# Kernel optimization log

Hardware: AMD Instinct MI355X
Metric: run time of the kernel (lower is better)

The kernel has to match this reference:

```python
import jax, jax.numpy as jnp
import numpy as np

N, H_IN, W_IN, D_OUT = 4, 512, 360, 512


def _ramp_filter(H):
    # fourier_fbp_filter(..., 'ramp') -> time domain, fftshifted, then reversed
    f = np.fft.fftfreq(H).reshape(-1, 1)
    fourier_filter = 2.0 * np.abs(f)
    time_filter = np.fft.fftshift(np.fft.ifft(fourier_filter, axis=0).real)
    time_filter = time_filter[::-1].copy()  # list-reverse in the original
    return time_filter.reshape(1, 1, H, 1).astype(np.float32)  # OIHW


def _backproj_ty(H, W, D):
    # y-coordinate of the grid_sample grid; x-coordinate exactly selects column i
    th = np.pi / 180.0 * np.linspace(0.0, 180.0, W, endpoint=False)  # [W]
    X, Y = np.mgrid[0:D, 0:D]
    xpr = (X - D // 2).astype(np.float64)
    ypr = (Y - D // 2).astype(np.float64)
    t = ypr[None] * np.cos(th)[:, None, None] - xpr[None] * np.sin(th)[:, None, None]
    return (t / (H // 2)).astype(np.float32)  # [W, D, D], in grid_sample coords


def setup_inputs() -> dict:
    key = jax.random.key(0)
    radon_image = jax.random.normal(key, (N, 1, H_IN, W_IN), dtype=jnp.float32)
    hG = jnp.asarray(_ramp_filter(H_IN))
    t_y = jnp.asarray(_backproj_ty(H_IN, W_IN, D_OUT))
    return {"radon_image": radon_image, "hG": hG, "t_y": t_y}


def _forward(radon_image, hG, t_y):
    Nb, _, H, W = radon_image.shape
    hH = H // 2
    padded = jnp.concatenate([radon_image, radon_image, radon_image], axis=2)  # [N,1,3H,W]
    filt = jax.lax.conv_general_dilated(
        padded, hG, window_strides=(1, 1), padding="VALID",
        dimension_numbers=("NCHW", "OIHW", "NCHW"))  # [N,1,2H+1,W]
    filt = filt[:, 0, hH + 1 : hH + H + 1, :]  # [N,H,W]

    cols = jnp.transpose(filt, (2, 0, 1))  # [W, N, H]: column i = angle i

    def body(acc, xs):
        col, ty = xs  # col: [N,H], ty: [D,D]
        # bilinear grid_sample along y, align_corners=True, zeros padding
        py = (ty + 1.0) * 0.5 * (H - 1)
        y0 = jnp.floor(py)
        fy = py - y0
        y0i = y0.astype(jnp.int32)
        y1i = y0i + 1
        w0 = jnp.where((y0i >= 0) & (y0i < H), 1.0 - fy, 0.0)
        w1 = jnp.where((y1i >= 0) & (y1i < H), fy, 0.0)
        v = col[:, jnp.clip(y0i, 0, H - 1)] * w0[None] \
          + col[:, jnp.clip(y1i, 0, H - 1)] * w1[None]  # [N,D,D]
        return acc + v, None

    D = t_y.shape[1]
    acc0 = jnp.zeros((Nb, D, D), dtype=filt.dtype)
    acc, _ = jax.lax.scan(body, acc0, (cols, t_y))
    return (acc * (np.pi / (2.0 * W)))[:, None]  # [N,1,D,D]


def reference(radon_image, hG, t_y):
    return _forward(radon_image, hG, t_y)
```

## Files before the change

### kernel.cpp

```cpp
#include <hip/hip_runtime.h>

#define HH 512
#define WW 360
#define NB 4
#define DD 512

#define NCHUNK 12
#define ANG_PER 30

#define FSTRIDE 768
#define FOFFS   128
#define NR      128

#define OFF_TAB  0
#define OFF_RT   1024
#define OFF_FILT (1024 + NB*WW*HH)
#define OFF_PART (OFF_FILT + (WW+1)*FSTRIDE*4)
#define CHUNK_ELEMS (NB*DD*DD)

#define GLOAD_LDS16(gp, lp)                                                   \
    __builtin_amdgcn_global_load_lds(                                         \
        (const __attribute__((address_space(1))) void*)(gp),                  \
        (__attribute__((address_space(3))) void*)(lp), 16, 0, 0)

__global__ __launch_bounds__(256) void k_transpose(const float* __restrict__ radon,
                                                   float* __restrict__ ws) {
    __shared__ float tile[32][33];
    int n  = blockIdx.z;
    int w0 = blockIdx.x * 32, h0 = blockIdx.y * 32;
    int x = threadIdx.x, y = threadIdx.y;
    const float* rn = radon + n * (HH * WW);
#pragma unroll
    for (int r = 0; r < 32; r += 8) {
        int h = h0 + y + r, w = w0 + x;
        tile[y + r][x] = (w < WW) ? rn[h * WW + w] : 0.f;
    }
    __syncthreads();
    float* rt = ws + OFF_RT + n * (WW * HH);
#pragma unroll
    for (int r = 0; r < 32; r += 8) {
        int w = w0 + y + r, h = h0 + x;
        if (w < WW) rt[w * HH + h] = tile[x][y + r];
    }
}

__global__ __launch_bounds__(256) void k_filter(const float* __restrict__ hG,
                                                float* __restrict__ ws) {
    __shared__ float r2[NB][1024];
    int wA  = blockIdx.x;
    int tid = threadIdx.x;

    if (tid == 0) {
        double th = (3.14159265358979323846 / 180.0) * (0.5 * (double)wA);
        double c = cos(th), s = sin(th);
        float2 ab;
        ab.x = (float)(c * (255.5 / 256.0));
        ab.y = (float)(-s * (255.5 / 256.0));
        ((float2*)(ws + OFF_TAB))[wA] = ab;
    }
    {
        float4* fp = (float4*)(ws + OFF_FILT) + (size_t)wA * FSTRIDE;
        float4 z = make_float4(0.f, 0.f, 0.f, 0.f);
        if (tid < 128) { fp[tid] = z; fp[640 + tid] = z; }
    }

    const float* rt = ws + OFF_RT;
    for (int t = tid; t < NB * 1024; t += 256) {
        int n = t >> 10, i = t & 1023;
        r2[n][i] = rt[(n * WW + wA) * HH + ((i + 257) & 511)];
    }
    __syncthreads();

    int n = tid >> 6, lane = tid & 63, y0 = lane << 3;
    float acc[8] = {0, 0, 0, 0, 0, 0, 0, 0};
    const float* rr = &r2[n][y0];
    float4 Wr0 = *(const float4*)(rr + 0);
    float4 Wr1 = *(const float4*)(rr + 4);
    float4 Wr2 = *(const float4*)(rr + 8);
    float4 Wr3 = *(const float4*)(rr + 12);

    for (int d = 0; d < 512; d += 8) {
        float hg[8];
#pragma unroll
        for (int q = 0; q < 8; ++q) hg[q] = hG[d + q];
        float wf[16] = {Wr0.x, Wr0.y, Wr0.z, Wr0.w, Wr1.x, Wr1.y, Wr1.z, Wr1.w,
                        Wr2.x, Wr2.y, Wr2.z, Wr2.w, Wr3.x, Wr3.y, Wr3.z, Wr3.w};
#pragma unroll
        for (int du = 0; du < 8; ++du)
#pragma unroll
            for (int u = 0; u < 8; ++u)
                acc[u] = fmaf(wf[du + u], hg[du], acc[u]);
        if (d < 504) {
            Wr0 = Wr2; Wr1 = Wr3;
            Wr2 = *(const float4*)(rr + d + 16);
            Wr3 = *(const float4*)(rr + d + 20);
        }
    }
    float* filt = ws + OFF_FILT;
#pragma unroll
    for (int u = 0; u < 8; ++u)
        filt[((size_t)wA * FSTRIDE + FOFFS + y0 + u) * 4 + n] = acc[u];
}

__global__ __launch_bounds__(256, 6) void k_backproj(const float* __restrict__ ws,
                                                     float* __restrict__ parts) {
    __shared__ float4 buf[2][NR];
    const int tid   = threadIdx.x;
    const int lane  = tid & 63;
    const int ithr  = tid >> 6;
    const int j     = blockIdx.x * 64 + lane;
    const int i0    = blockIdx.y * 32 + ithr;
    const int chunk = blockIdx.z;

    const float2* tab = (const float2*)(ws + OFF_TAB);
    const float4* fd  = (const float4*)(ws + OFF_FILT);

    float acc[8][4];
#pragma unroll
    for (int u = 0; u < 8; ++u)
#pragma unroll
        for (int n = 0; n < 4; ++n) acc[u][n] = 0.f;

    float jf = (float)(j - 256);
    float ifl[8];
#pragma unroll
    for (int u = 0; u < 8; ++u) ifl[u] = (float)(i0 + 4 * u - 256);

    const float jlo = (float)((int)blockIdx.x * 64 - 256);
    const float jhi = (float)((int)blockIdx.x * 64 + 63 - 256);
    const float ilo = (float)((int)blockIdx.y * 32 - 256);
    const float ihi = (float)((int)blockIdx.y * 32 + 31 - 256);

    const int wbeg = chunk * ANG_PER;
    float2 abc = tab[wbeg];
    float2 abn = tab[wbeg + 1];

    float basefc;
    {
        float t = fminf(fmaf(abc.x, jlo, 255.5f), fmaf(abc.x, jhi, 255.5f));
        float pymin = fminf(fmaf(abc.y, ilo, t), fmaf(abc.y, ihi, t));
        basefc = floorf(pymin) - 2.0f;
    }
    if (tid < NR)
        GLOAD_LDS16(fd + (size_t)wbeg * FSTRIDE + (FOFFS + (int)basefc + tid),
                    &buf[0][tid]);
    __syncthreads();

    int cur = 0;
    for (int k = 0; k < ANG_PER; ++k) {
        const int w = wbeg + k;
        float2 abn2 = tab[min(w + 2, WW - 1)];
        float basefn = 0.f;
        if (k + 1 < ANG_PER) {
            float t = fminf(fmaf(abn.x, jlo, 255.5f), fmaf(abn.x, jhi, 255.5f));
            float pymin = fminf(fmaf(abn.y, ilo, t), fmaf(abn.y, ihi, t));
            basefn = floorf(pymin) - 2.0f;
            if (tid < NR)
                GLOAD_LDS16(fd + (size_t)(w + 1) * FSTRIDE + (FOFFS + (int)basefn + tid),
                            &buf[cur ^ 1][tid]);
        }

        float pybase = fmaf(abc.x, jf, 255.5f);
        const float4* cb = buf[cur];
#pragma unroll
        for (int u = 0; u < 8; ++u) {
            float pya = fmaf(abc.y, ifl[u], pybase);
            float pyr = pya - basefc;
            float cf  = truncf(pyr);
            float fy  = pyr - cf;
            int   c   = (int)cf;
            float4 p0 = cb[c];
            float4 p1 = cb[c + 1];
            float w0  = 1.f - fy;
            acc[u][0] = fmaf(p1.x, fy, fmaf(p0.x, w0, acc[u][0]));
            acc[u][1] = fmaf(p1.y, fy, fmaf(p0.y, w0, acc[u][1]));
            acc[u][2] = fmaf(p1.z, fy, fmaf(p0.z, w0, acc[u][2]));
            acc[u][3] = fmaf(p1.w, fy, fmaf(p0.w, w0, acc[u][3]));
        }
        __syncthreads();
        abc = abn; abn = abn2; basefc = basefn; cur ^= 1;
    }

    float* part = parts + (size_t)chunk * CHUNK_ELEMS;
#pragma unroll
    for (int n = 0; n < 4; ++n)
#pragma unroll
        for (int u = 0; u < 8; ++u)
            part[(n * DD + (i0 + 4 * u)) * DD + j] = acc[u][n];
}

__global__ __launch_bounds__(256) void k_reduce(float* __restrict__ out,
                                                const float* __restrict__ ws) {
    int t = blockIdx.x * 256 + threadIdx.x;
    const float4* p = (const float4*)(ws + OFF_PART);
    const int C4 = CHUNK_ELEMS / 4;
    float4 a = p[t];
#pragma unroll
    for (int c = 1; c < NCHUNK; ++c) {
        float4 b = p[t + c * C4];
        a.x += b.x; a.y += b.y; a.z += b.z; a.w += b.w;
    }
    const float s = (float)(3.14159265358979323846 / 720.0);
    float4 r;
    r.x = a.x * s; r.y = a.y * s; r.z = a.z * s; r.w = a.w * s;
    ((float4*)out)[t] = r;
}

extern "C" void kernel_launch(void* const* d_in, const int* in_sizes, int n_in,
                              void* d_out, int out_size, void* d_ws, size_t ws_size,
                              hipStream_t stream) {
    const float* radon = (const float*)d_in[0];
    const float* hG    = (const float*)d_in[1];
    float* out = (float*)d_out;
    float* ws  = (float*)d_ws;

    k_transpose<<<dim3(12, 16, 4), dim3(32, 8), 0, stream>>>(radon, ws);
    k_filter<<<WW, 256, 0, stream>>>(hG, ws);
    k_backproj<<<dim3(8, 16, NCHUNK), 256, 0, stream>>>(ws, ws + OFF_PART);
    k_reduce<<<1024, 256, 0, stream>>>(out, ws);
}
```

Measured before the change: 109.4 us.

## Deepen backprojection LDS prefetch to four-stage ring with partial vmcnt waits

The backprojection kernel now prefetches filtered columns three angles ahead into a four-slot LDS ring, instead of double buffering with a full __syncthreads each angle. It waits with s_waitcnt vmcnt(2) and a raw barrier so two loads stay in flight. The per-chunk angle table is also staged into LDS once, replacing a global load per iteration. This aims to hide global-to-LDS latency, at the cost of doubled LDS use and fragile manual counter accounting, since threads with tid>=128 issue no loads.

```diff
diff --git a/kernel.cpp b/kernel.cpp
--- a/kernel.cpp
+++ b/kernel.cpp
@@ -104,16 +104,21 @@
 
 __global__ __launch_bounds__(256, 6) void k_backproj(const float* __restrict__ ws,
                                                      float* __restrict__ parts) {
-    __shared__ float4 buf[2][NR];
+    __shared__ float4 buf[4][NR];
+    __shared__ float2 tl[ANG_PER];
     const int tid   = threadIdx.x;
     const int lane  = tid & 63;
     const int ithr  = tid >> 6;
     const int j     = blockIdx.x * 64 + lane;
     const int i0    = blockIdx.y * 32 + ithr;
     const int chunk = blockIdx.z;
+    const int wbeg  = chunk * ANG_PER;
 
     const float2* tab = (const float2*)(ws + OFF_TAB);
     const float4* fd  = (const float4*)(ws + OFF_FILT);
+
+    if (tid < ANG_PER) tl[tid] = tab[wbeg + tid];
+    __syncthreads();
 
     float acc[8][4];
 #pragma unroll
@@ -131,41 +136,44 @@
     const float ilo = (float)((int)blockIdx.y * 32 - 256);
     const float ihi = (float)((int)blockIdx.y * 32 + 31 - 256);
 
-    const int wbeg = chunk * ANG_PER;
-    float2 abc = tab[wbeg];
-    float2 abn = tab[wbeg + 1];
-
-    float basefc;
-    {
-        float t = fminf(fmaf(abc.x, jlo, 255.5f), fmaf(abc.x, jhi, 255.5f));
-        float pymin = fminf(fmaf(abc.y, ilo, t), fmaf(abc.y, ihi, t));
-        basefc = floorf(pymin) - 2.0f;
-    }
-    if (tid < NR)
-        GLOAD_LDS16(fd + (size_t)wbeg * FSTRIDE + (FOFFS + (int)basefc + tid),
-                    &buf[0][tid]);
-    __syncthreads();
-
-    int cur = 0;
+#define CALC_BASE(ab, dst)                                                    \
+    {                                                                         \
+        float t_ = fminf(fmaf((ab).x, jlo, 255.5f), fmaf((ab).x, jhi, 255.5f)); \
+        float pm_ = fminf(fmaf((ab).y, ilo, t_), fmaf((ab).y, ihi, t_));      \
+        (dst) = floorf(pm_) - 2.0f;                                           \
+    }
+
+    float2 abA = tl[0], abB = tl[1], abC = tl[2], abD;
+    float bA, bB, bC, bD;
+    CALC_BASE(abA, bA); CALC_BASE(abB, bB); CALC_BASE(abC, bC);
+
+    if (tid < NR) {
+        GLOAD_LDS16(fd + (size_t)(wbeg + 0) * FSTRIDE + (FOFFS + (int)bA + tid), &buf[0][tid]);
+        GLOAD_LDS16(fd + (size_t)(wbeg + 1) * FSTRIDE + (FOFFS + (int)bB + tid), &buf[1][tid]);
+        GLOAD_LDS16(fd + (size_t)(wbeg + 2) * FSTRIDE + (FOFFS + (int)bC + tid), &buf[2][tid]);
+    }
+    asm volatile("s_waitcnt vmcnt(2)" ::: "memory");
+    __builtin_amdgcn_s_barrier();
+    __builtin_amdgcn_sched_barrier(0);
+
     for (int k = 0; k < ANG_PER; ++k) {
-        const int w = wbeg + k;
-        float2 abn2 = tab[min(w + 2, WW - 1)];
-        float basefn = 0.f;
-        if (k + 1 < ANG_PER) {
-            float t = fminf(fmaf(abn.x, jlo, 255.5f), fmaf(abn.x, jhi, 255.5f));
-            float pymin = fminf(fmaf(abn.y, ilo, t), fmaf(abn.y, ihi, t));
-            basefn = floorf(pymin) - 2.0f;
+        {
+            bool ok  = (k + 3 < ANG_PER);
+            int  idx = ok ? (k + 3) : 0;
+            abD = tl[idx];
+            if (ok) { CALC_BASE(abD, bD); } else { bD = 0.0f; }
+            int wsrc = ok ? (wbeg + k + 3) : wbeg;
             if (tid < NR)
-                GLOAD_LDS16(fd + (size_t)(w + 1) * FSTRIDE + (FOFFS + (int)basefn + tid),
-                            &buf[cur ^ 1][tid]);
+                GLOAD_LDS16(fd + (size_t)wsrc * FSTRIDE + (FOFFS + (int)bD + tid),
+                            &buf[(k + 3) & 3][tid]);
         }
 
-        float pybase = fmaf(abc.x, jf, 255.5f);
-        const float4* cb = buf[cur];
+        float pybase = fmaf(abA.x, jf, 255.5f);
+        const float4* cb = buf[k & 3];
 #pragma unroll
         for (int u = 0; u < 8; ++u) {
-            float pya = fmaf(abc.y, ifl[u], pybase);
-            float pyr = pya - basefc;
+            float pya = fmaf(abA.y, ifl[u], pybase);
+            float pyr = pya - bA;
             float cf  = truncf(pyr);
             float fy  = pyr - cf;
             int   c   = (int)cf;
@@ -177,9 +185,16 @@
             acc[u][2] = fmaf(p1.z, fy, fmaf(p0.z, w0, acc[u][2]));
             acc[u][3] = fmaf(p1.w, fy, fmaf(p0.w, w0, acc[u][3]));
         }
-        __syncthreads();
-        abc = abn; abn = abn2; basefc = basefn; cur ^= 1;
-    }
+
+        asm volatile("s_waitcnt vmcnt(2)" ::: "memory");
+        __builtin_amdgcn_s_barrier();
+        __builtin_amdgcn_sched_barrier(0);
+
+        abA = abB; abB = abC; abC = abD;
+        bA  = bB;  bB  = bC;  bC  = bD;
+    }
+
+    asm volatile("s_waitcnt vmcnt(0)" ::: "memory");
 
     float* part = parts + (size_t)chunk * CHUNK_ELEMS;
 #pragma unroll
@@ -187,6 +202,7 @@
 #pragma unroll
         for (int u = 0; u < 8; ++u)
             part[(n * DD + (i0 + 4 * u)) * DD + j] = acc[u][n];
+#undef CALC_BASE
 }
 
 __global__ __launch_bounds__(256) void k_reduce(float* __restrict__ out,
```

Measured after the change: 108.2 us. No clear change (-1.1%).
